# Kernel tuning notes

Measured on AMD Instinct MI355X. Metric: run time of the kernel, lower is better.

## Reference

```python
import jax, jax.numpy as jnp
import numpy as np

N_NODES = 100000
EMBED_DIM = 128
HIDDEN = 64
N_EDGES = 1000000


def setup_inputs() -> dict:
    key = jax.random.key(0)
    k_z, k_e1, k_e2, k_w1, k_w2 = jax.random.split(key, 5)
    Z = jax.random.normal(k_z, (N_NODES, EMBED_DIM), dtype=jnp.float32)
    edge_index = jnp.stack([
        jax.random.randint(k_e1, (N_EDGES,), 0, N_NODES, dtype=jnp.int64 if jax.config.jax_enable_x64 else jnp.int32),
        jax.random.randint(k_e2, (N_EDGES,), 0, N_NODES, dtype=jnp.int64 if jax.config.jax_enable_x64 else jnp.int32),
    ], axis=0)
    # Xavier-uniform init as in _reset_parameters; weights stored [in, out]
    lim1 = float(np.sqrt(6.0 / (2 * EMBED_DIM + HIDDEN)))
    W1 = jax.random.uniform(k_w1, (2 * EMBED_DIM, HIDDEN), minval=-lim1, maxval=lim1, dtype=jnp.float32)
    b1 = jnp.zeros((HIDDEN,), dtype=jnp.float32)
    lim2 = float(np.sqrt(6.0 / (HIDDEN + 1)))
    W2 = jax.random.uniform(k_w2, (HIDDEN, 1), minval=-lim2, maxval=lim2, dtype=jnp.float32)
    b2 = jnp.zeros((1,), dtype=jnp.float32)
    return {"Z": Z, "edge_index": edge_index, "W1": W1, "b1": b1, "W2": W2, "b2": b2}


def reference(Z, edge_index, W1, b1, W2, b2):
    src, dst = edge_index[0], edge_index[1]
    # concat([Z[src], Z[dst]]) @ W1 == Z[src] @ W1[:d] + Z[dst] @ W1[d:]
    # (avoids materializing the [E, 2d] pair tensor; same math)
    d = Z.shape[-1]
    h = Z[src] @ W1[:d] + Z[dst] @ W1[d:] + b1      # [E, hidden]
    h = jax.nn.relu(h)
    logits = h @ W2 + b2                              # [E, 1]
    return logits[:, 0]                               # [E]
```

## Files before the change

### kernel.cpp

```cpp
#include <hip/hip_runtime.h>
#include <hip/hip_bf16.h>

#define EMBED 128
#define HID   64

typedef unsigned short ushort;
typedef ushort ushort8 __attribute__((ext_vector_type(8)));

__device__ __forceinline__ float bf2f(ushort u) {
    union { unsigned int i; float f; } c;
    c.i = ((unsigned int)u) << 16;
    return c.f;
}
__device__ __forceinline__ ushort f2bf(float f) {
    union { float f; unsigned int i; } c;
    c.f = f;
    unsigned int r = c.i + 0x7FFFu + ((c.i >> 16) & 1u);
    return (ushort)(r >> 16);
}

__global__ __launch_bounds__(256, 2)
void node_proj_kernel(const float* __restrict__ Z, const float* __restrict__ W1,
                      const float* __restrict__ b1, ushort* __restrict__ P,
                      int n_nodes) {
    __shared__ float w2s[128 * 128];
    __shared__ float zt[128 * 32];

    const int t = threadIdx.x;

    for (int idx = t; idx < 128 * 128; idx += 256) {
        const int k = idx >> 7, jj = idx & 127;
        w2s[idx] = (jj < HID) ? W1[k * HID + jj]
                              : W1[(EMBED + k) * HID + (jj - HID)];
    }

    const int tj = t & 15;
    const int tn = t >> 4;
    const int j0 = tj * 8;
    const int base = blockIdx.x * 128;
    const int myswz = 8 * (tn & 3);

    float bh[8];
#pragma unroll
    for (int c = 0; c < 8; ++c) bh[c] = 0.5f * b1[(j0 + c) & (HID - 1)];

    const int sr = t >> 3;
    const int sc = t & 7;

    float acc[8][8];
#pragma unroll
    for (int i = 0; i < 8; ++i)
#pragma unroll
        for (int c = 0; c < 8; ++c) acc[i][c] = 0.f;

    for (int it = 0; it < 4; ++it) {
        const int k0 = it * 32;

#pragma unroll
        for (int s = 0; s < 4; ++s) {
            const int r = sr + 32 * s;
            int gn = base + r;
            if (gn >= n_nodes) gn = n_nodes - 1;
            const float4 g = *(const float4*)(Z + (size_t)gn * EMBED + k0 + sc * 4);
            const int pc = (sc * 4) ^ (8 * ((r >> 3) & 3));
            *(float4*)(&zt[r * 32 + pc]) = g;
        }
        __syncthreads();

#pragma unroll 2
        for (int k = 0; k < 32; ++k) {
            const float4 wv0 = *(const float4*)(&w2s[(k0 + k) * 128 + j0]);
            const float4 wv1 = *(const float4*)(&w2s[(k0 + k) * 128 + j0 + 4]);
            const int zc = k ^ myswz;
            float zv[8];
#pragma unroll
            for (int i = 0; i < 8; ++i)
                zv[i] = zt[(tn * 8 + i) * 32 + zc];
#pragma unroll
            for (int i = 0; i < 8; ++i) {
                acc[i][0] = fmaf(zv[i], wv0.x, acc[i][0]);
                acc[i][1] = fmaf(zv[i], wv0.y, acc[i][1]);
                acc[i][2] = fmaf(zv[i], wv0.z, acc[i][2]);
                acc[i][3] = fmaf(zv[i], wv0.w, acc[i][3]);
                acc[i][4] = fmaf(zv[i], wv1.x, acc[i][4]);
                acc[i][5] = fmaf(zv[i], wv1.y, acc[i][5]);
                acc[i][6] = fmaf(zv[i], wv1.z, acc[i][6]);
                acc[i][7] = fmaf(zv[i], wv1.w, acc[i][7]);
            }
        }
        __syncthreads();
    }

#pragma unroll
    for (int i = 0; i < 8; ++i) {
        const int n = base + tn * 8 + i;
        if (n < n_nodes) {
            ushort8 pk;
#pragma unroll
            for (int c = 0; c < 8; ++c) pk[c] = f2bf(acc[i][c] + bh[c]);
            *(ushort8*)(P + (size_t)n * 128 + j0) = pk;
        }
    }
}

__global__ __launch_bounds__(256)
void edge_mlp_kernel(const ushort* __restrict__ P, const int* __restrict__ src,
                     const int* __restrict__ dst, const float* __restrict__ W2,
                     const float* __restrict__ b2, float* __restrict__ out,
                     int n_edges) {
    const int gtid  = blockIdx.x * 256 + threadIdx.x;
    const int lane8 = gtid & 7;
    const int e     = gtid >> 3;
    if (e >= n_edges) return;

    const float4 w2a = *(const float4*)(W2 + lane8 * 8);
    const float4 w2b = *(const float4*)(W2 + lane8 * 8 + 4);

    const int s = src[e];
    const int d = dst[e];
    const ushort8 ps = *(const ushort8*)(P + (size_t)s * 128 + lane8 * 8);
    const ushort8 pd = *(const ushort8*)(P + (size_t)d * 128 + HID + lane8 * 8);

    float part;
    {
        const float h0 = fmaxf(bf2f(ps[0]) + bf2f(pd[0]), 0.f);
        const float h1 = fmaxf(bf2f(ps[1]) + bf2f(pd[1]), 0.f);
        const float h2 = fmaxf(bf2f(ps[2]) + bf2f(pd[2]), 0.f);
        const float h3 = fmaxf(bf2f(ps[3]) + bf2f(pd[3]), 0.f);
        const float h4 = fmaxf(bf2f(ps[4]) + bf2f(pd[4]), 0.f);
        const float h5 = fmaxf(bf2f(ps[5]) + bf2f(pd[5]), 0.f);
        const float h6 = fmaxf(bf2f(ps[6]) + bf2f(pd[6]), 0.f);
        const float h7 = fmaxf(bf2f(ps[7]) + bf2f(pd[7]), 0.f);
        part = h0 * w2a.x + h1 * w2a.y + h2 * w2a.z + h3 * w2a.w
             + h4 * w2b.x + h5 * w2b.y + h6 * w2b.z + h7 * w2b.w;
    }

    part += __shfl_xor(part, 4, 8);
    part += __shfl_xor(part, 2, 8);
    part += __shfl_xor(part, 1, 8);

    if (lane8 == 0) out[e] = part + b2[0];
}

__global__ __launch_bounds__(256)
void edge_direct_kernel(const float* __restrict__ Z, const int* __restrict__ src,
                        const int* __restrict__ dst, const float* __restrict__ W1,
                        const float* __restrict__ b1, const float* __restrict__ W2,
                        const float* __restrict__ b2, float* __restrict__ out,
                        int n_edges) {
    __shared__ float w1s[2 * EMBED * HID];
    for (int i = threadIdx.x; i < 2 * EMBED * HID; i += 256) w1s[i] = W1[i];
    __syncthreads();

    const int gtid   = blockIdx.x * 256 + threadIdx.x;
    const int lane16 = gtid & 15;
    const int e      = gtid >> 4;
    if (e >= n_edges) return;

    const int s = src[e];
    const int d = dst[e];
    const float* zs = Z + (size_t)s * EMBED;
    const float* zd = Z + (size_t)d * EMBED;

    float h[4] = {b1[lane16 * 4 + 0], b1[lane16 * 4 + 1],
                  b1[lane16 * 4 + 2], b1[lane16 * 4 + 3]};
    for (int k = 0; k < EMBED; ++k) {
        const float zsk = zs[k];
        const float zdk = zd[k];
        const float4 w1a = *(const float4*)(&w1s[k * HID + lane16 * 4]);
        const float4 w1b = *(const float4*)(&w1s[(EMBED + k) * HID + lane16 * 4]);
        h[0] = fmaf(zsk, w1a.x, fmaf(zdk, w1b.x, h[0]));
        h[1] = fmaf(zsk, w1a.y, fmaf(zdk, w1b.y, h[1]));
        h[2] = fmaf(zsk, w1a.z, fmaf(zdk, w1b.z, h[2]));
        h[3] = fmaf(zsk, w1a.w, fmaf(zdk, w1b.w, h[3]));
    }

    const float4 w2v = *(const float4*)(W2 + lane16 * 4);
    float part = fmaxf(h[0], 0.f) * w2v.x + fmaxf(h[1], 0.f) * w2v.y +
                 fmaxf(h[2], 0.f) * w2v.z + fmaxf(h[3], 0.f) * w2v.w;
    part += __shfl_xor(part, 8, 16);
    part += __shfl_xor(part, 4, 16);
    part += __shfl_xor(part, 2, 16);
    part += __shfl_xor(part, 1, 16);

    if (lane16 == 0) out[e] = part + b2[0];
}

extern "C" void kernel_launch(void* const* d_in, const int* in_sizes, int n_in,
                              void* d_out, int out_size, void* d_ws, size_t ws_size,
                              hipStream_t stream) {
    const float* Z  = (const float*)d_in[0];
    const int*   EI = (const int*)d_in[1];
    const float* W1 = (const float*)d_in[2];
    const float* b1 = (const float*)d_in[3];
    const float* W2 = (const float*)d_in[4];
    const float* b2 = (const float*)d_in[5];
    float* out = (float*)d_out;

    const int n_nodes = in_sizes[0] / EMBED;
    const int E       = in_sizes[1] / 2;

    const size_t p_bytes = (size_t)n_nodes * (2 * HID) * sizeof(ushort);

    if (ws_size >= p_bytes) {
        ushort* P = (ushort*)d_ws;
        const int node_blocks = (n_nodes + 127) / 128;
        node_proj_kernel<<<node_blocks, 256, 0, stream>>>(Z, W1, b1, P, n_nodes);

        const int edge_blocks = (E * 8 + 255) / 256;
        edge_mlp_kernel<<<edge_blocks, 256, 0, stream>>>(
            P, EI, EI + E, W2, b2, out, E);
    } else {
        const int edge_blocks = (E * 16 + 255) / 256;
        edge_direct_kernel<<<edge_blocks, 256, 0, stream>>>(
            Z, EI, EI + E, W1, b1, W2, b2, out, E);
    }
}
```

Before: 175.8 us.

## Transpose node tile in LDS for vector reads and batch four edges per group

The node projection GEMM now stores the Z tile transposed (k-major) with an XOR swizzle, so each thread reads its 8 node values as two float4 LDS loads instead of 8 scalar loads. The output columns are split into two groups of four, at j and 64+j, which changes the store pattern. The edge kernel has each 8-lane group handle four edges strided by a quarter of E, issuing all index and P gathers up front to raise memory-level parallelism. The cost is more registers and scattered scalar LDS writes during the transpose.

Measured after the change: 174.9 us. No clear change (-0.5%).

```diff
diff --git a/kernel.cpp b/kernel.cpp
--- a/kernel.cpp
+++ b/kernel.cpp
@@ -6,6 +6,7 @@
 
 typedef unsigned short ushort;
 typedef ushort ushort8 __attribute__((ext_vector_type(8)));
+typedef ushort ushort4_t __attribute__((ext_vector_type(4)));
 
 __device__ __forceinline__ float bf2f(ushort u) {
     union { unsigned int i; float f; } c;
@@ -24,7 +25,7 @@
                       const float* __restrict__ b1, ushort* __restrict__ P,
                       int n_nodes) {
     __shared__ float w2s[128 * 128];
-    __shared__ float zt[128 * 32];
+    __shared__ float zt[32 * 128];
 
     const int t = threadIdx.x;
 
@@ -36,16 +37,16 @@
 
     const int tj = t & 15;
     const int tn = t >> 4;
-    const int j0 = tj * 8;
+    const int jA = tj * 4;
     const int base = blockIdx.x * 128;
-    const int myswz = 8 * (tn & 3);
-
-    float bh[8];
-#pragma unroll
-    for (int c = 0; c < 8; ++c) bh[c] = 0.5f * b1[(j0 + c) & (HID - 1)];
+
+    float bh[4];
+#pragma unroll
+    for (int c = 0; c < 4; ++c) bh[c] = 0.5f * b1[jA + c];
 
     const int sr = t >> 3;
     const int sc = t & 7;
+    const int wswz = 8 * (sc & 3);
 
     float acc[8][8];
 #pragma unroll
@@ -62,30 +63,45 @@
             int gn = base + r;
             if (gn >= n_nodes) gn = n_nodes - 1;
             const float4 g = *(const float4*)(Z + (size_t)gn * EMBED + k0 + sc * 4);
-            const int pc = (sc * 4) ^ (8 * ((r >> 3) & 3));
-            *(float4*)(&zt[r * 32 + pc]) = g;
+            const int col = r ^ wswz;
+            zt[(sc * 4 + 0) * 128 + col] = g.x;
+            zt[(sc * 4 + 1) * 128 + col] = g.y;
+            zt[(sc * 4 + 2) * 128 + col] = g.z;
+            zt[(sc * 4 + 3) * 128 + col] = g.w;
         }
         __syncthreads();
 
-#pragma unroll 2
+#pragma unroll 4
         for (int k = 0; k < 32; ++k) {
-            const float4 wv0 = *(const float4*)(&w2s[(k0 + k) * 128 + j0]);
-            const float4 wv1 = *(const float4*)(&w2s[(k0 + k) * 128 + j0 + 4]);
-            const int zc = k ^ myswz;
-            float zv[8];
-#pragma unroll
-            for (int i = 0; i < 8; ++i)
-                zv[i] = zt[(tn * 8 + i) * 32 + zc];
-#pragma unroll
-            for (int i = 0; i < 8; ++i) {
-                acc[i][0] = fmaf(zv[i], wv0.x, acc[i][0]);
-                acc[i][1] = fmaf(zv[i], wv0.y, acc[i][1]);
-                acc[i][2] = fmaf(zv[i], wv0.z, acc[i][2]);
-                acc[i][3] = fmaf(zv[i], wv0.w, acc[i][3]);
-                acc[i][4] = fmaf(zv[i], wv1.x, acc[i][4]);
-                acc[i][5] = fmaf(zv[i], wv1.y, acc[i][5]);
-                acc[i][6] = fmaf(zv[i], wv1.z, acc[i][6]);
-                acc[i][7] = fmaf(zv[i], wv1.w, acc[i][7]);
+            const float4 wv0 = *(const float4*)(&w2s[(k0 + k) * 128 + jA]);
+            const float4 wv1 = *(const float4*)(&w2s[(k0 + k) * 128 + 64 + jA]);
+            const int zb = 8 * (tn ^ ((k >> 2) & 3));
+            const float4 z0 = *(const float4*)(&zt[k * 128 + zb]);
+            const float4 z1 = *(const float4*)(&zt[k * 128 + zb + 4]);
+
+#pragma unroll
+            for (int i = 0; i < 4; ++i) {
+                const float zi = (i == 0) ? z0.x : (i == 1) ? z0.y : (i == 2) ? z0.z : z0.w;
+                acc[i][0] = fmaf(zi, wv0.x, acc[i][0]);
+                acc[i][1] = fmaf(zi, wv0.y, acc[i][1]);
+                acc[i][2] = fmaf(zi, wv0.z, acc[i][2]);
+                acc[i][3] = fmaf(zi, wv0.w, acc[i][3]);
+                acc[i][4] = fmaf(zi, wv1.x, acc[i][4]);
+                acc[i][5] = fmaf(zi, wv1.y, acc[i][5]);
+                acc[i][6] = fmaf(zi, wv1.z, acc[i][6]);
+                acc[i][7] = fmaf(zi, wv1.w, acc[i][7]);
+            }
+#pragma unroll
+            for (int i = 4; i < 8; ++i) {
+                const float zi = (i == 4) ? z1.x : (i == 5) ? z1.y : (i == 6) ? z1.z : z1.w;
+                acc[i][0] = fmaf(zi, wv0.x, acc[i][0]);
+                acc[i][1] = fmaf(zi, wv0.y, acc[i][1]);
+                acc[i][2] = fmaf(zi, wv0.z, acc[i][2]);
+                acc[i][3] = fmaf(zi, wv0.w, acc[i][3]);
+                acc[i][4] = fmaf(zi, wv1.x, acc[i][4]);
+                acc[i][5] = fmaf(zi, wv1.y, acc[i][5]);
+                acc[i][6] = fmaf(zi, wv1.z, acc[i][6]);
+                acc[i][7] = fmaf(zi, wv1.w, acc[i][7]);
             }
         }
         __syncthreads();
@@ -95,10 +111,14 @@
     for (int i = 0; i < 8; ++i) {
         const int n = base + tn * 8 + i;
         if (n < n_nodes) {
-            ushort8 pk;
-#pragma unroll
-            for (int c = 0; c < 8; ++c) pk[c] = f2bf(acc[i][c] + bh[c]);
-            *(ushort8*)(P + (size_t)n * 128 + j0) = pk;
+            ushort4_t pa, pb;
+#pragma unroll
+            for (int c = 0; c < 4; ++c) {
+                pa[c] = f2bf(acc[i][c] + bh[c]);
+                pb[c] = f2bf(acc[i][c + 4] + bh[c]);
+            }
+            *(ushort4_t*)(P + (size_t)n * 128 + jA)      = pa;
+            *(ushort4_t*)(P + (size_t)n * 128 + 64 + jA) = pb;
         }
     }
 }
@@ -110,36 +130,59 @@
                      int n_edges) {
     const int gtid  = blockIdx.x * 256 + threadIdx.x;
     const int lane8 = gtid & 7;
-    const int e     = gtid >> 3;
-    if (e >= n_edges) return;
+    const int g     = gtid >> 3;
+    const int quarter = (n_edges + 3) >> 2;
+    if (g >= quarter) return;
 
     const float4 w2a = *(const float4*)(W2 + lane8 * 8);
     const float4 w2b = *(const float4*)(W2 + lane8 * 8 + 4);
 
-    const int s = src[e];
-    const int d = dst[e];
-    const ushort8 ps = *(const ushort8*)(P + (size_t)s * 128 + lane8 * 8);
-    const ushort8 pd = *(const ushort8*)(P + (size_t)d * 128 + HID + lane8 * 8);
-
-    float part;
-    {
-        const float h0 = fmaxf(bf2f(ps[0]) + bf2f(pd[0]), 0.f);
-        const float h1 = fmaxf(bf2f(ps[1]) + bf2f(pd[1]), 0.f);
-        const float h2 = fmaxf(bf2f(ps[2]) + bf2f(pd[2]), 0.f);
-        const float h3 = fmaxf(bf2f(ps[3]) + bf2f(pd[3]), 0.f);
-        const float h4 = fmaxf(bf2f(ps[4]) + bf2f(pd[4]), 0.f);
-        const float h5 = fmaxf(bf2f(ps[5]) + bf2f(pd[5]), 0.f);
-        const float h6 = fmaxf(bf2f(ps[6]) + bf2f(pd[6]), 0.f);
-        const float h7 = fmaxf(bf2f(ps[7]) + bf2f(pd[7]), 0.f);
-        part = h0 * w2a.x + h1 * w2a.y + h2 * w2a.z + h3 * w2a.w
-             + h4 * w2b.x + h5 * w2b.y + h6 * w2b.z + h7 * w2b.w;
-    }
-
-    part += __shfl_xor(part, 4, 8);
-    part += __shfl_xor(part, 2, 8);
-    part += __shfl_xor(part, 1, 8);
-
-    if (lane8 == 0) out[e] = part + b2[0];
+    int e[4];  bool ok[4];
+    int s[4], d[4];
+#pragma unroll
+    for (int m = 0; m < 4; ++m) {
+        e[m] = g + m * quarter;
+        ok[m] = e[m] < n_edges;
+        const int ec = ok[m] ? e[m] : 0;
+        s[m] = src[ec];
+        d[m] = dst[ec];
+    }
+
+    ushort8 ps[4], pd[4];
+#pragma unroll
+    for (int m = 0; m < 4; ++m) {
+        ps[m] = *(const ushort8*)(P + (size_t)s[m] * 128 + lane8 * 8);
+        pd[m] = *(const ushort8*)(P + (size_t)d[m] * 128 + HID + lane8 * 8);
+    }
+
+    float part[4];
+#pragma unroll
+    for (int m = 0; m < 4; ++m) {
+        const float h0 = fmaxf(bf2f(ps[m][0]) + bf2f(pd[m][0]), 0.f);
+        const float h1 = fmaxf(bf2f(ps[m][1]) + bf2f(pd[m][1]), 0.f);
+        const float h2 = fmaxf(bf2f(ps[m][2]) + bf2f(pd[m][2]), 0.f);
+        const float h3 = fmaxf(bf2f(ps[m][3]) + bf2f(pd[m][3]), 0.f);
+        const float h4 = fmaxf(bf2f(ps[m][4]) + bf2f(pd[m][4]), 0.f);
+        const float h5 = fmaxf(bf2f(ps[m][5]) + bf2f(pd[m][5]), 0.f);
+        const float h6 = fmaxf(bf2f(ps[m][6]) + bf2f(pd[m][6]), 0.f);
+        const float h7 = fmaxf(bf2f(ps[m][7]) + bf2f(pd[m][7]), 0.f);
+        part[m] = h0 * w2a.x + h1 * w2a.y + h2 * w2a.z + h3 * w2a.w
+                + h4 * w2b.x + h5 * w2b.y + h6 * w2b.z + h7 * w2b.w;
+    }
+
+#pragma unroll
+    for (int m = 0; m < 4; ++m) {
+        part[m] += __shfl_xor(part[m], 4, 8);
+        part[m] += __shfl_xor(part[m], 2, 8);
+        part[m] += __shfl_xor(part[m], 1, 8);
+    }
+
+    if (lane8 == 0) {
+        const float bb = b2[0];
+#pragma unroll
+        for (int m = 0; m < 4; ++m)
+            if (ok[m]) out[e[m]] = part[m] + bb;
+    }
 }
 
 __global__ __launch_bounds__(256)
@@ -207,7 +250,8 @@
         const int node_blocks = (n_nodes + 127) / 128;
         node_proj_kernel<<<node_blocks, 256, 0, stream>>>(Z, W1, b1, P, n_nodes);
 
-        const int edge_blocks = (E * 8 + 255) / 256;
+        const int quarter = (E + 3) >> 2;
+        const int edge_blocks = (quarter * 8 + 255) / 256;
         edge_mlp_kernel<<<edge_blocks, 256, 0, stream>>>(
             P, EI, EI + E, W2, b2, out, E);
     } else {
```

## Move node projection GEMM to bf16 MFMA with split-precision hi/lo terms

Applied to the files above, without the earlier changes.

Replaces the FP32 FMA tile GEMM in the node projection with MFMA 16x16x32 bf16 instructions. Both Z and W1 are split into bf16 high and low parts, and three MFMAs per tile keep close to FP32 accuracy. A small prep kernel lays out the W1 fragments in workspace, and each block copies them into shared memory. This targets the ALU-bound node GEMM stage, at the cost of an extra launch, uncoalesced scalar 2-byte stores of P, and more workspace.

Measured after the change: 141.8 us. 1.24x faster.

```diff
diff --git a/kernel.cpp b/kernel.cpp
--- a/kernel.cpp
+++ b/kernel.cpp
@@ -6,6 +6,8 @@
 
 typedef unsigned short ushort;
 typedef ushort ushort8 __attribute__((ext_vector_type(8)));
+typedef short  bf16x8  __attribute__((ext_vector_type(8)));
+typedef float  f32x4   __attribute__((ext_vector_type(4)));
 
 __device__ __forceinline__ float bf2f(ushort u) {
     union { unsigned int i; float f; } c;
@@ -19,86 +21,117 @@
     return (ushort)(r >> 16);
 }
 
+__global__ __launch_bounds__(256)
+void frag_prep_kernel(const float* __restrict__ W1, ushort* __restrict__ fragH,
+                      ushort* __restrict__ fragL) {
+    const int tid = blockIdx.x * 256 + threadIdx.x;
+    if (tid >= 2048) return;
+    const int lane = tid & 63;
+    const int kt   = (tid >> 6) & 3;
+    const int jt   = tid >> 8;
+    const int q    = lane >> 4;
+    const int m16  = lane & 15;
+
+    ushort8 fh, fl;
+#pragma unroll
+    for (int r = 0; r < 8; ++r) {
+        const int k = kt * 32 + q * 8 + r;
+        const int j = jt * 16 + m16;
+        const float v = (j < HID) ? W1[k * HID + j]
+                                  : W1[(EMBED + k) * HID + (j - HID)];
+        const ushort h = f2bf(v);
+        fh[r] = h;
+        fl[r] = f2bf(v - bf2f(h));
+    }
+    const int fi = (jt * 4 + kt) * 64 + lane;
+    *(ushort8*)(fragH + fi * 8) = fh;
+    *(ushort8*)(fragL + fi * 8) = fl;
+}
+
 __global__ __launch_bounds__(256, 2)
-void node_proj_kernel(const float* __restrict__ Z, const float* __restrict__ W1,
-                      const float* __restrict__ b1, ushort* __restrict__ P,
-                      int n_nodes) {
-    __shared__ float w2s[128 * 128];
-    __shared__ float zt[128 * 32];
+void node_proj_mfma(const float* __restrict__ Z, const ushort* __restrict__ fragH,
+                    const ushort* __restrict__ fragL, const float* __restrict__ b1,
+                    ushort* __restrict__ P, int n_nodes) {
+    __shared__ __align__(16) ushort sFH[32 * 64 * 8];
+    __shared__ __align__(16) ushort sFL[32 * 64 * 8];
 
     const int t = threadIdx.x;
 
-    for (int idx = t; idx < 128 * 128; idx += 256) {
-        const int k = idx >> 7, jj = idx & 127;
-        w2s[idx] = (jj < HID) ? W1[k * HID + jj]
-                              : W1[(EMBED + k) * HID + (jj - HID)];
-    }
-
-    const int tj = t & 15;
-    const int tn = t >> 4;
-    const int j0 = tj * 8;
-    const int base = blockIdx.x * 128;
-    const int myswz = 8 * (tn & 3);
-
-    float bh[8];
-#pragma unroll
-    for (int c = 0; c < 8; ++c) bh[c] = 0.5f * b1[(j0 + c) & (HID - 1)];
-
-    const int sr = t >> 3;
-    const int sc = t & 7;
-
-    float acc[8][8];
-#pragma unroll
-    for (int i = 0; i < 8; ++i)
-#pragma unroll
-        for (int c = 0; c < 8; ++c) acc[i][c] = 0.f;
-
-    for (int it = 0; it < 4; ++it) {
-        const int k0 = it * 32;
-
-#pragma unroll
-        for (int s = 0; s < 4; ++s) {
-            const int r = sr + 32 * s;
-            int gn = base + r;
-            if (gn >= n_nodes) gn = n_nodes - 1;
-            const float4 g = *(const float4*)(Z + (size_t)gn * EMBED + k0 + sc * 4);
-            const int pc = (sc * 4) ^ (8 * ((r >> 3) & 3));
-            *(float4*)(&zt[r * 32 + pc]) = g;
+    for (int i = t; i < 2048; i += 256) {
+        ((ushort8*)sFH)[i] = ((const ushort8*)fragH)[i];
+        ((ushort8*)sFL)[i] = ((const ushort8*)fragL)[i];
+    }
+
+    const int wave = t >> 6;
+    const int lane = t & 63;
+    const int q    = lane >> 4;
+    const int m16  = lane & 15;
+    const int n0   = blockIdx.x * 128 + wave * 32;
+
+    const int rA = n0 + m16;
+    const int rB = n0 + 16 + m16;
+    const float* gA = Z + (size_t)(rA < n_nodes ? rA : n_nodes - 1) * EMBED;
+    const float* gB = Z + (size_t)(rB < n_nodes ? rB : n_nodes - 1) * EMBED;
+
+    float b1h[4];
+#pragma unroll
+    for (int jm = 0; jm < 4; ++jm) b1h[jm] = 0.5f * b1[jm * 16 + m16];
+
+    __syncthreads();
+
+    f32x4 acc0[8], acc1[8];
+#pragma unroll
+    for (int jt = 0; jt < 8; ++jt) {
+        acc0[jt] = (f32x4){0.f, 0.f, 0.f, 0.f};
+        acc1[jt] = (f32x4){0.f, 0.f, 0.f, 0.f};
+    }
+
+    for (int kt = 0; kt < 4; ++kt) {
+        const int k0 = kt * 32 + q * 8;
+
+        float za[8], zb[8];
+        *(float4*)(za)     = *(const float4*)(gA + k0);
+        *(float4*)(za + 4) = *(const float4*)(gA + k0 + 4);
+        *(float4*)(zb)     = *(const float4*)(gB + k0);
+        *(float4*)(zb + 4) = *(const float4*)(gB + k0 + 4);
+
+        bf16x8 ah0, al0, ah1, al1;
+#pragma unroll
+        for (int r = 0; r < 8; ++r) {
+            const ushort h0 = f2bf(za[r]);
+            ah0[r] = (short)h0;
+            al0[r] = (short)f2bf(za[r] - bf2f(h0));
+            const ushort h1 = f2bf(zb[r]);
+            ah1[r] = (short)h1;
+            al1[r] = (short)f2bf(zb[r] - bf2f(h1));
         }
-        __syncthreads();
-
-#pragma unroll 2
-        for (int k = 0; k < 32; ++k) {
-            const float4 wv0 = *(const float4*)(&w2s[(k0 + k) * 128 + j0]);
-            const float4 wv1 = *(const float4*)(&w2s[(k0 + k) * 128 + j0 + 4]);
-            const int zc = k ^ myswz;
-            float zv[8];
-#pragma unroll
-            for (int i = 0; i < 8; ++i)
-                zv[i] = zt[(tn * 8 + i) * 32 + zc];
-#pragma unroll
-            for (int i = 0; i < 8; ++i) {
-                acc[i][0] = fmaf(zv[i], wv0.x, acc[i][0]);
-                acc[i][1] = fmaf(zv[i], wv0.y, acc[i][1]);
-                acc[i][2] = fmaf(zv[i], wv0.z, acc[i][2]);
-                acc[i][3] = fmaf(zv[i], wv0.w, acc[i][3]);
-                acc[i][4] = fmaf(zv[i], wv1.x, acc[i][4]);
-                acc[i][5] = fmaf(zv[i], wv1.y, acc[i][5]);
-                acc[i][6] = fmaf(zv[i], wv1.z, acc[i][6]);
-                acc[i][7] = fmaf(zv[i], wv1.w, acc[i][7]);
-            }
+
+#pragma unroll
+        for (int jt = 0; jt < 8; ++jt) {
+            const int fi = (jt * 4 + kt) * 64 + lane;
+            const bf16x8 bh = ((const bf16x8*)sFH)[fi];
+            const bf16x8 bl = ((const bf16x8*)sFL)[fi];
+
+            acc0[jt] = __builtin_amdgcn_mfma_f32_16x16x32_bf16(ah0, bh, acc0[jt], 0, 0, 0);
+            acc0[jt] = __builtin_amdgcn_mfma_f32_16x16x32_bf16(al0, bh, acc0[jt], 0, 0, 0);
+            acc0[jt] = __builtin_amdgcn_mfma_f32_16x16x32_bf16(ah0, bl, acc0[jt], 0, 0, 0);
+
+            acc1[jt] = __builtin_amdgcn_mfma_f32_16x16x32_bf16(ah1, bh, acc1[jt], 0, 0, 0);
+            acc1[jt] = __builtin_amdgcn_mfma_f32_16x16x32_bf16(al1, bh, acc1[jt], 0, 0, 0);
+            acc1[jt] = __builtin_amdgcn_mfma_f32_16x16x32_bf16(ah1, bl, acc1[jt], 0, 0, 0);
         }
-        __syncthreads();
-    }
-
-#pragma unroll
-    for (int i = 0; i < 8; ++i) {
-        const int n = base + tn * 8 + i;
-        if (n < n_nodes) {
-            ushort8 pk;
-#pragma unroll
-            for (int c = 0; c < 8; ++c) pk[c] = f2bf(acc[i][c] + bh[c]);
-            *(ushort8*)(P + (size_t)n * 128 + j0) = pk;
+    }
+
+#pragma unroll
+    for (int jt = 0; jt < 8; ++jt) {
+        const int col = jt * 16 + m16;
+        const float bb = b1h[jt & 3];
+#pragma unroll
+        for (int r = 0; r < 4; ++r) {
+            const int ra = n0 + q * 4 + r;
+            if (ra < n_nodes) P[(size_t)ra * 128 + col] = f2bf(acc0[jt][r] + bb);
+            const int rb = n0 + 16 + q * 4 + r;
+            if (rb < n_nodes) P[(size_t)rb * 128 + col] = f2bf(acc1[jt][r] + bb);
         }
     }
 }
@@ -200,12 +233,18 @@
     const int n_nodes = in_sizes[0] / EMBED;
     const int E       = in_sizes[1] / 2;
 
-    const size_t p_bytes = (size_t)n_nodes * (2 * HID) * sizeof(ushort);
-
-    if (ws_size >= p_bytes) {
-        ushort* P = (ushort*)d_ws;
+    const size_t p_bytes    = (size_t)n_nodes * (2 * HID) * sizeof(ushort);
+    const size_t frag_bytes = 32 * 64 * 8 * sizeof(ushort);
+
+    if (ws_size >= p_bytes + 2 * frag_bytes) {
+        ushort* P     = (ushort*)d_ws;
+        ushort* fragH = (ushort*)((char*)d_ws + p_bytes);
+        ushort* fragL = (ushort*)((char*)d_ws + p_bytes + frag_bytes);
+
+        frag_prep_kernel<<<8, 256, 0, stream>>>(W1, fragH, fragL);
+
         const int node_blocks = (n_nodes + 127) / 128;
-        node_proj_kernel<<<node_blocks, 256, 0, stream>>>(Z, W1, b1, P, n_nodes);
+        node_proj_mfma<<<node_blocks, 256, 0, stream>>>(Z, fragH, fragL, b1, P, n_nodes);
 
         const int edge_blocks = (E * 8 + 255) / 256;
         edge_mlp_kernel<<<edge_blocks, 256, 0, stream>>>(
```
